# Performance work log

Hardware: AMD Instinct MI355X
Metric: run time of the kernel (lower is better)

## Reference

```python
import math
import jax, jax.numpy as jnp
import numpy as np

H = 16  # num_attention_heads
D = 64  # attention_head_size
ALPHA = 32.0  # PB-relax alpha


def setup_inputs() -> dict:
    key = jax.random.key(0)
    ks = jax.random.split(key, 8)
    B, S, C = 4, 1024, 1024
    scale = 1.0 / math.sqrt(C)
    return {
        "hidden_states": jax.random.normal(ks[0], (B, S, C), jnp.float32),
        "attention_mask": jnp.zeros((B, 1, 1, S), jnp.float32),
        "rel_pos": jax.random.normal(ks[1], (B, H, S, S), jnp.float32),
        "rel_2d_pos": jax.random.normal(ks[2], (B, H, S, S), jnp.float32),
        "Wq": jax.random.normal(ks[3], (C, C), jnp.float32) * scale,
        "bq": jnp.zeros((C,), jnp.float32),
        "Wk": jax.random.normal(ks[4], (C, C), jnp.float32) * scale,
        "bk": jnp.zeros((C,), jnp.float32),
        "Wv": jax.random.normal(ks[5], (C, C), jnp.float32) * scale,
        "bv": jnp.zeros((C,), jnp.float32),
    }


def _heads(x, B, S):
    # [B,S,C] -> [B,H,S,D]
    return x.reshape(B, S, H, D).transpose(0, 2, 1, 3)


def cogview_softmax(scores):
    # PB-relax: softmax(((s/alpha) - max(s/alpha)) * alpha)
    s = scores / ALPHA
    m = jnp.max(s, axis=-1, keepdims=True)
    return jax.nn.softmax((s - m) * ALPHA, axis=-1)


def reference(hidden_states, attention_mask, rel_pos, rel_2d_pos,
              Wq, bq, Wk, bk, Wv, bv):
    B, S, C = hidden_states.shape
    inv_sqrt_d = 1.0 / math.sqrt(D)
    # torch nn.Linear: y = x @ W.T + b; here W is stored as [out, in]
    q = _heads(hidden_states @ Wq.T + bq, B, S)  # [B,H,S,D]
    k = _heads(hidden_states @ Wk.T + bk, B, S)
    v = _heads(hidden_states @ Wv.T + bv, B, S)

    scores = jnp.einsum('bhqd,bhkd->bhqk', q * inv_sqrt_d, k)
    scores = scores + (rel_pos + rel_2d_pos) * inv_sqrt_d
    scores = scores + attention_mask  # broadcast [B,1,1,S]

    probs = cogview_softmax(scores)  # dropout prob = 0 (eval)
    ctx = jnp.einsum('bhqk,bhkd->bhqd', probs, v)
    ctx = ctx.transpose(0, 2, 1, 3).reshape(B, S, C)
    return ctx
```

## Files before the change

kernel.cpp:

```cpp
#include <hip/hip_runtime.h>
#include <hip/hip_bf16.h>

typedef __attribute__((ext_vector_type(8))) short bf16x8;
typedef __attribute__((ext_vector_type(4))) float f32x4;

#define LDSG(g, l) __builtin_amdgcn_global_load_lds(                      \
    (const __attribute__((address_space(1))) void*)(g),                   \
    (__attribute__((address_space(3))) void*)(l), 16, 0, 0)

#define LOG2E 1.44269504088896f
#define RELSC 0.180336880111112f

__global__ __launch_bounds__(256) void cvt_kernel(
    const float* __restrict__ hs,
    const float* __restrict__ wq, const float* __restrict__ wk,
    const float* __restrict__ wv,
    __hip_bfloat16* __restrict__ hbf, __hip_bfloat16* __restrict__ wbf)
{
  const int NH = (4 * 1024 * 1024) / 4;
  const int NW = (1024 * 1024) / 4;
  int i = blockIdx.x * 256 + threadIdx.x;
  float4 v;
  __hip_bfloat16* dst;
  if (i < NH) {
    v = ((const float4*)hs)[i];
    dst = hbf + (size_t)i * 4;
  } else {
    int j = i - NH;
    int which = j / NW, r = j - which * NW;
    const float* src = which == 0 ? wq : (which == 1 ? wk : wv);
    v = ((const float4*)src)[r];
    dst = wbf + (size_t)j * 4;
  }
  union { ushort4 u; __hip_bfloat16 b[4]; } o;
  o.b[0] = __float2bfloat16(v.x);
  o.b[1] = __float2bfloat16(v.y);
  o.b[2] = __float2bfloat16(v.z);
  o.b[3] = __float2bfloat16(v.w);
  *((ushort4*)dst) = o.u;
}

__global__ __launch_bounds__(256) void qkv_gemm(
    const __hip_bfloat16* __restrict__ A,
    const __hip_bfloat16* __restrict__ W,
    const float* __restrict__ bq, const float* __restrict__ bk,
    const float* __restrict__ bv,
    __hip_bfloat16* __restrict__ qo, __hip_bfloat16* __restrict__ ko,
    __hip_bfloat16* __restrict__ vo)
{
  const int K = 1024;
  __shared__ __hip_bfloat16 As[128 * 64];
  __shared__ __hip_bfloat16 Bs[128 * 64];
  const int bid = blockIdx.x;
  const int bm = bid & 31, bn = bid >> 5;
  const int m0 = bm * 128, n0 = bn * 128;
  const int tid = threadIdx.x, wid = tid >> 6, lane = tid & 63;
  const int wm = wid >> 1, wn = wid & 1;

  f32x4 acc[4][4] = {};

  const int srow = lane >> 3;
  const int schunk = (lane & 7) ^ srow;

  for (int k0 = 0; k0 < K; k0 += 64) {
#pragma unroll
    for (int p = 0; p < 4; ++p) {
      int r = (wid * 4 + p) * 8 + srow;
      LDSG(&A[(size_t)(m0 + r) * K + k0 + schunk * 8], &As[(wid * 4 + p) * 512]);
      LDSG(&W[(size_t)(n0 + r) * K + k0 + schunk * 8], &Bs[(wid * 4 + p) * 512]);
    }
    __syncthreads();
#pragma unroll
    for (int ks = 0; ks < 2; ++ks) {
      bf16x8 af[4], bfr[4];
#pragma unroll
      for (int mi = 0; mi < 4; ++mi) {
        int row = wm * 64 + mi * 16 + (lane & 15);
        int slot = (ks * 4 + (lane >> 4)) ^ (lane & 7);
        af[mi] = *(const bf16x8*)((const char*)As + row * 128 + slot * 16);
      }
#pragma unroll
      for (int ni = 0; ni < 4; ++ni) {
        int row = wn * 64 + ni * 16 + (lane & 15);
        int slot = (ks * 4 + (lane >> 4)) ^ (lane & 7);
        bfr[ni] = *(const bf16x8*)((const char*)Bs + row * 128 + slot * 16);
      }
#pragma unroll
      for (int mi = 0; mi < 4; ++mi)
#pragma unroll
        for (int ni = 0; ni < 4; ++ni)
          acc[mi][ni] = __builtin_amdgcn_mfma_f32_16x16x32_bf16(
              af[mi], bfr[ni], acc[mi][ni], 0, 0, 0);
    }
    __syncthreads();
  }

#pragma unroll
  for (int ni = 0; ni < 4; ++ni) {
    int n = n0 + wn * 64 + ni * 16 + (lane & 15);
    int which = n >> 10;
    int h = (n >> 6) & 15;
    int d = n & 63;
    const float* bias = which == 0 ? bq : (which == 1 ? bk : bv);
    float bval = bias[n & 1023];
    if (which == 2) {
#pragma unroll
      for (int mi = 0; mi < 4; ++mi) {
        int m = m0 + wm * 64 + mi * 16 + (lane >> 4) * 4;
        int b = m >> 10, s = m & 1023;
        union { ushort4 u; __hip_bfloat16 bb[4]; } o;
#pragma unroll
        for (int j = 0; j < 4; ++j)
          o.bb[j] = __float2bfloat16(acc[mi][ni][j] + bval);
        *(ushort4*)&vo[((size_t)((b * 16 + h) * 64 + d) << 10) + s] = o.u;
      }
    } else {
      __hip_bfloat16* dst = which == 0 ? qo : ko;
      float scale = (which == 0) ? RELSC : 1.0f;
#pragma unroll
      for (int mi = 0; mi < 4; ++mi) {
#pragma unroll
        for (int j = 0; j < 4; ++j) {
          int m = m0 + wm * 64 + mi * 16 + (lane >> 4) * 4 + j;
          int b = m >> 10, s = m & 1023;
          float val = (acc[mi][ni][j] + bval) * scale;
          dst[(((size_t)(b * 16 + h) << 10) + s) * 64 + d] = __float2bfloat16(val);
        }
      }
    }
  }
}

__global__ __launch_bounds__(256, 3) void attn_kernel(
    const __hip_bfloat16* __restrict__ qg, const __hip_bfloat16* __restrict__ kg,
    const __hip_bfloat16* __restrict__ vtg,
    const float* __restrict__ rel1, const float* __restrict__ rel2,
    const float* __restrict__ mask, float* __restrict__ out)
{
  __shared__ __hip_bfloat16 Ks[2][64 * 64];
  __shared__ __hip_bfloat16 Vts[2][64 * 64];
  __shared__ __hip_bfloat16 Ps[4][16 * 64];

  const int bid = blockIdx.x;
  const int bh = bid & 63, qt = bid >> 6;
  const int b = bh >> 4, h = bh & 15;
  const int tid = threadIdx.x, wid = tid >> 6, lane = tid & 63;
  const int lg = lane >> 4, ln15 = lane & 15;

  const size_t kvbase = (size_t)bh << 16;
  const int q0 = qt * 64 + wid * 16;

  bf16x8 qf[2];
  qf[0] = *(const bf16x8*)&qg[kvbase + (size_t)(q0 + ln15) * 64 + lg * 8];
  qf[1] = *(const bf16x8*)&qg[kvbase + (size_t)(q0 + ln15) * 64 + 32 + lg * 8];

  f32x4 accO[4] = {};
  float mrun = -1e30f, lrun = 0.f;

  const int srow = lane >> 3, sc8 = lane & 7;
  const float* relp1 = rel1 + ((size_t)bh << 20) + (size_t)(q0 + ln15) * 1024;
  const float* relp2 = rel2 + ((size_t)bh << 20) + (size_t)(q0 + ln15) * 1024;
  const float* maskp = mask + ((size_t)b << 10);

  float4 ra[2][2][4];

#define REL_LOAD(BUF, KB) do {                                              \
    _Pragma("unroll") for (int ct = 0; ct < 4; ++ct) {                      \
      ra[BUF][0][ct] = *(const float4*)&relp1[(KB) + ct * 16 + lg * 4];     \
      ra[BUF][1][ct] = *(const float4*)&relp2[(KB) + ct * 16 + lg * 4];     \
    } } while (0)

#define STAGE(BUF, KB) do {                                                 \
    _Pragma("unroll") for (int pp = 0; pp < 2; ++pp) {                      \
      int rr = (wid * 2 + pp) * 8 + srow;                                   \
      LDSG(&kg[kvbase + (size_t)((KB) + rr) * 64 + (sc8 ^ (rr & 7)) * 8],   \
           &Ks[BUF][(wid * 2 + pp) * 512]);                                 \
      LDSG(&vtg[kvbase + (size_t)rr * 1024 + (KB) + (sc8 ^ (rr & 7)) * 8],  \
           &Vts[BUF][(wid * 2 + pp) * 512]);                                \
    } } while (0)

#define BODY(CB, KT) do {                                                   \
    if ((KT) + 1 < 16) {                                                    \
      REL_LOAD((CB) ^ 1, ((KT) + 1) * 64);                                  \
      STAGE((CB) ^ 1, ((KT) + 1) * 64);                                     \
    }                                                                       \
    f32x4 st[4] = {};                                                       \
    _Pragma("unroll") for (int ks = 0; ks < 2; ++ks)                        \
      _Pragma("unroll") for (int ct = 0; ct < 4; ++ct) {                    \
        int row = ct * 16 + ln15;                                           \
        bf16x8 kf = *(const bf16x8*)((const char*)&Ks[CB][0] + row * 128 +  \
                                     (((ks * 4 + lg) ^ (row & 7)) * 16));   \
        st[ct] = __builtin_amdgcn_mfma_f32_16x16x32_bf16(kf, qf[ks], st[ct],\
                                                         0, 0, 0);          \
      }                                                                     \
    float p[4][4]; float mt = -1e30f;                                       \
    const int kb_ = (KT) * 64;                                              \
    _Pragma("unroll") for (int ct = 0; ct < 4; ++ct) {                      \
      float4 mv = *(const float4*)&maskp[kb_ + ct * 16 + lg * 4];           \
      _Pragma("unroll") for (int j = 0; j < 4; ++j) {                       \
        float sv = st[ct][j] +                                              \
                   RELSC * (((const float*)&ra[CB][0][ct])[j] +             \
                            ((const float*)&ra[CB][1][ct])[j]) +            \
                   LOG2E * ((const float*)&mv)[j];                          \
        p[ct][j] = sv; mt = fmaxf(mt, sv);                                  \
      }                                                                     \
    }                                                                       \
    mt = fmaxf(mt, __shfl_xor(mt, 16, 64));                                 \
    mt = fmaxf(mt, __shfl_xor(mt, 32, 64));                                 \
    float mnew = fmaxf(mrun, mt);                                           \
    float sc_ = __builtin_amdgcn_exp2f(mrun - mnew);                        \
    mrun = mnew;                                                            \
    float lsum = 0.f;                                                       \
    _Pragma("unroll") for (int ct = 0; ct < 4; ++ct)                        \
      _Pragma("unroll") for (int j = 0; j < 4; ++j) {                       \
        float e = __builtin_amdgcn_exp2f(p[ct][j] - mnew);                  \
        p[ct][j] = e; lsum += e;                                            \
      }                                                                     \
    lsum += __shfl_xor(lsum, 16, 64);                                       \
    lsum += __shfl_xor(lsum, 32, 64);                                       \
    lrun = lrun * sc_ + lsum;                                               \
    _Pragma("unroll") for (int dt = 0; dt < 4; ++dt) accO[dt] *= sc_;       \
    __hip_bfloat16* Pw = &Ps[wid][0];                                       \
    _Pragma("unroll") for (int ct = 0; ct < 4; ++ct) {                      \
      union { ushort4 u; __hip_bfloat16 bb[4]; } w;                         \
      _Pragma("unroll") for (int j = 0; j < 4; ++j)                         \
        w.bb[j] = __float2bfloat16(p[ct][j]);                               \
      *(ushort4*)((char*)Pw + ln15 * 128 +                                  \
                  ((ct * 32 + lg * 8) ^ ((ln15 & 7) << 4))) = w.u;          \
    }                                                                       \
    bf16x8 pt[2];                                                           \
    pt[0] = *(const bf16x8*)((const char*)Pw + ln15 * 128 +                 \
                             ((lg * 16) ^ ((ln15 & 7) << 4)));              \
    pt[1] = *(const bf16x8*)((const char*)Pw + ln15 * 128 +                 \
                             ((64 + lg * 16) ^ ((ln15 & 7) << 4)));         \
    _Pragma("unroll") for (int ks = 0; ks < 2; ++ks)                        \
      _Pragma("unroll") for (int dt = 0; dt < 4; ++dt) {                    \
        int drow = dt * 16 + ln15;                                          \
        bf16x8 vf = *(const bf16x8*)((const char*)&Vts[CB][0] + drow * 128 +\
                                     (((ks * 4 + lg) ^ (drow & 7)) * 16));  \
        accO[dt] = __builtin_amdgcn_mfma_f32_16x16x32_bf16(vf, pt[ks],      \
                                                           accO[dt], 0, 0, 0);\
      }                                                                     \
    __syncthreads();                                                        \
  } while (0)

  REL_LOAD(0, 0);
  STAGE(0, 0);
  __syncthreads();

  for (int t = 0; t < 8; ++t) {
    BODY(0, 2 * t);
    BODY(1, 2 * t + 1);
  }

  float rl = 1.0f / lrun;
#pragma unroll
  for (int dt = 0; dt < 4; ++dt) {
    float4 o;
    o.x = accO[dt][0] * rl;
    o.y = accO[dt][1] * rl;
    o.z = accO[dt][2] * rl;
    o.w = accO[dt][3] * rl;
    *(float4*)&out[((size_t)(b * 1024 + q0 + ln15)) * 1024 + h * 64 +
                   dt * 16 + lg * 4] = o;
  }
}

extern "C" void kernel_launch(void* const* d_in, const int* in_sizes, int n_in,
                              void* d_out, int out_size, void* d_ws,
                              size_t ws_size, hipStream_t stream) {
  const float* hs   = (const float*)d_in[0];
  const float* mask = (const float*)d_in[1];
  const float* rel1 = (const float*)d_in[2];
  const float* rel2 = (const float*)d_in[3];
  const float* Wq   = (const float*)d_in[4];
  const float* bq   = (const float*)d_in[5];
  const float* Wk   = (const float*)d_in[6];
  const float* bk   = (const float*)d_in[7];
  const float* Wv   = (const float*)d_in[8];
  const float* bv   = (const float*)d_in[9];

  char* ws = (char*)d_ws;
  __hip_bfloat16* hbf = (__hip_bfloat16*)(ws);
  __hip_bfloat16* wbf = (__hip_bfloat16*)(ws + 8388608);
  __hip_bfloat16* qb  = (__hip_bfloat16*)(ws + 14680064);
  __hip_bfloat16* kb  = (__hip_bfloat16*)(ws + 23068672);
  __hip_bfloat16* vtb = (__hip_bfloat16*)(ws + 31457280);

  cvt_kernel<<<7168, 256, 0, stream>>>(hs, Wq, Wk, Wv, hbf, wbf);
  qkv_gemm<<<768, 256, 0, stream>>>(hbf, wbf, bq, bk, bv, qb, kb, vtb);
  attn_kernel<<<1024, 256, 0, stream>>>(qb, kb, vtb, rel1, rel2, mask,
                                        (float*)d_out);
}
```

Before: 205.6 us.

## Use single-wave attention blocks loading K and V directly into registers

The attention kernel changes from 4-wave blocks with K and V staged through LDS to 64-thread blocks, each handling 16 query rows. K and V fragments now come straight from global memory into registers, with K and the relative-position bias register double-buffered across tiles. This removes LDS staging and the per-tile __syncthreads. The cost is that each wave fetches its own copy of K and V instead of sharing it, which raises global and L2 traffic and register pressure.

```diff
diff --git a/kernel.cpp b/kernel.cpp
--- a/kernel.cpp
+++ b/kernel.cpp
@@ -131,24 +131,22 @@
   }
 }
 
-__global__ __launch_bounds__(256, 3) void attn_kernel(
+__global__ __launch_bounds__(64, 2) void attn_kernel(
     const __hip_bfloat16* __restrict__ qg, const __hip_bfloat16* __restrict__ kg,
     const __hip_bfloat16* __restrict__ vtg,
     const float* __restrict__ rel1, const float* __restrict__ rel2,
     const float* __restrict__ mask, float* __restrict__ out)
 {
-  __shared__ __hip_bfloat16 Ks[2][64 * 64];
-  __shared__ __hip_bfloat16 Vts[2][64 * 64];
-  __shared__ __hip_bfloat16 Ps[4][16 * 64];
+  __shared__ __hip_bfloat16 Ps[16 * 64];
 
   const int bid = blockIdx.x;
   const int bh = bid & 63, qt = bid >> 6;
   const int b = bh >> 4, h = bh & 15;
-  const int tid = threadIdx.x, wid = tid >> 6, lane = tid & 63;
+  const int lane = threadIdx.x;
   const int lg = lane >> 4, ln15 = lane & 15;
 
   const size_t kvbase = (size_t)bh << 16;
-  const int q0 = qt * 64 + wid * 16;
+  const int q0 = qt * 16;
 
   bf16x8 qf[2];
   qf[0] = *(const bf16x8*)&qg[kvbase + (size_t)(q0 + ln15) * 64 + lg * 8];
@@ -157,50 +155,49 @@
   f32x4 accO[4] = {};
   float mrun = -1e30f, lrun = 0.f;
 
-  const int srow = lane >> 3, sc8 = lane & 7;
   const float* relp1 = rel1 + ((size_t)bh << 20) + (size_t)(q0 + ln15) * 1024;
   const float* relp2 = rel2 + ((size_t)bh << 20) + (size_t)(q0 + ln15) * 1024;
   const float* maskp = mask + ((size_t)b << 10);
 
-  float4 ra[2][2][4];
-
-#define REL_LOAD(BUF, KB) do {                                              \
+#define LOAD_REL(R1, R2, KBO) do {                                          \
     _Pragma("unroll") for (int ct = 0; ct < 4; ++ct) {                      \
-      ra[BUF][0][ct] = *(const float4*)&relp1[(KB) + ct * 16 + lg * 4];     \
-      ra[BUF][1][ct] = *(const float4*)&relp2[(KB) + ct * 16 + lg * 4];     \
+      R1[ct] = *(const float4*)&relp1[(KBO) + ct * 16 + lg * 4];            \
+      R2[ct] = *(const float4*)&relp2[(KBO) + ct * 16 + lg * 4];            \
     } } while (0)
 
-#define STAGE(BUF, KB) do {                                                 \
-    _Pragma("unroll") for (int pp = 0; pp < 2; ++pp) {                      \
-      int rr = (wid * 2 + pp) * 8 + srow;                                   \
-      LDSG(&kg[kvbase + (size_t)((KB) + rr) * 64 + (sc8 ^ (rr & 7)) * 8],   \
-           &Ks[BUF][(wid * 2 + pp) * 512]);                                 \
-      LDSG(&vtg[kvbase + (size_t)rr * 1024 + (KB) + (sc8 ^ (rr & 7)) * 8],  \
-           &Vts[BUF][(wid * 2 + pp) * 512]);                                \
-    } } while (0)
-
-#define BODY(CB, KT) do {                                                   \
-    if ((KT) + 1 < 16) {                                                    \
-      REL_LOAD((CB) ^ 1, ((KT) + 1) * 64);                                  \
-      STAGE((CB) ^ 1, ((KT) + 1) * 64);                                     \
+#define LOAD_K(KF, KBO) do {                                                \
+    _Pragma("unroll") for (int ks = 0; ks < 2; ++ks)                        \
+      _Pragma("unroll") for (int ct = 0; ct < 4; ++ct)                      \
+        KF[ks * 4 + ct] = *(const bf16x8*)&kg[kvbase +                      \
+            (size_t)((KBO) + ct * 16 + ln15) * 64 + ks * 32 + lg * 8];      \
+    } while (0)
+
+#define LOAD_V(VF, KBO) do {                                                \
+    _Pragma("unroll") for (int ks = 0; ks < 2; ++ks)                        \
+      _Pragma("unroll") for (int dt = 0; dt < 4; ++dt)                      \
+        VF[ks * 4 + dt] = *(const bf16x8*)&vtg[kvbase +                     \
+            (size_t)(dt * 16 + ln15) * 1024 + (KBO) + ks * 32 + lg * 8];    \
+    } while (0)
+
+#define BODY(RC1, RC2, KC, RN1, RN2, KN, KT) do {                           \
+    bf16x8 vfr[8];                                                          \
+    LOAD_V(vfr, (KT) * 64);                                                 \
+    if ((KT) < 15) {                                                        \
+      LOAD_REL(RN1, RN2, ((KT) + 1) * 64);                                  \
+      LOAD_K(KN, ((KT) + 1) * 64);                                          \
     }                                                                       \
     f32x4 st[4] = {};                                                       \
     _Pragma("unroll") for (int ks = 0; ks < 2; ++ks)                        \
-      _Pragma("unroll") for (int ct = 0; ct < 4; ++ct) {                    \
-        int row = ct * 16 + ln15;                                           \
-        bf16x8 kf = *(const bf16x8*)((const char*)&Ks[CB][0] + row * 128 +  \
-                                     (((ks * 4 + lg) ^ (row & 7)) * 16));   \
-        st[ct] = __builtin_amdgcn_mfma_f32_16x16x32_bf16(kf, qf[ks], st[ct],\
-                                                         0, 0, 0);          \
-      }                                                                     \
+      _Pragma("unroll") for (int ct = 0; ct < 4; ++ct)                      \
+        st[ct] = __builtin_amdgcn_mfma_f32_16x16x32_bf16(                   \
+            KC[ks * 4 + ct], qf[ks], st[ct], 0, 0, 0);                      \
     float p[4][4]; float mt = -1e30f;                                       \
-    const int kb_ = (KT) * 64;                                              \
     _Pragma("unroll") for (int ct = 0; ct < 4; ++ct) {                      \
-      float4 mv = *(const float4*)&maskp[kb_ + ct * 16 + lg * 4];           \
+      float4 mv = *(const float4*)&maskp[(KT) * 64 + ct * 16 + lg * 4];     \
       _Pragma("unroll") for (int j = 0; j < 4; ++j) {                       \
         float sv = st[ct][j] +                                              \
-                   RELSC * (((const float*)&ra[CB][0][ct])[j] +             \
-                            ((const float*)&ra[CB][1][ct])[j]) +            \
+                   RELSC * (((const float*)&RC1[ct])[j] +                   \
+                            ((const float*)&RC2[ct])[j]) +                  \
                    LOG2E * ((const float*)&mv)[j];                          \
         p[ct][j] = sv; mt = fmaxf(mt, sv);                                  \
       }                                                                     \
@@ -220,37 +217,34 @@
     lsum += __shfl_xor(lsum, 32, 64);                                       \
     lrun = lrun * sc_ + lsum;                                               \
     _Pragma("unroll") for (int dt = 0; dt < 4; ++dt) accO[dt] *= sc_;       \
-    __hip_bfloat16* Pw = &Ps[wid][0];                                       \
     _Pragma("unroll") for (int ct = 0; ct < 4; ++ct) {                      \
       union { ushort4 u; __hip_bfloat16 bb[4]; } w;                         \
       _Pragma("unroll") for (int j = 0; j < 4; ++j)                         \
         w.bb[j] = __float2bfloat16(p[ct][j]);                               \
-      *(ushort4*)((char*)Pw + ln15 * 128 +                                  \
+      *(ushort4*)((char*)Ps + ln15 * 128 +                                  \
                   ((ct * 32 + lg * 8) ^ ((ln15 & 7) << 4))) = w.u;          \
     }                                                                       \
     bf16x8 pt[2];                                                           \
-    pt[0] = *(const bf16x8*)((const char*)Pw + ln15 * 128 +                 \
+    pt[0] = *(const bf16x8*)((const char*)Ps + ln15 * 128 +                 \
                              ((lg * 16) ^ ((ln15 & 7) << 4)));              \
-    pt[1] = *(const bf16x8*)((const char*)Pw + ln15 * 128 +                 \
+    pt[1] = *(const bf16x8*)((const char*)Ps + ln15 * 128 +                 \
                              ((64 + lg * 16) ^ ((ln15 & 7) << 4)));         \
     _Pragma("unroll") for (int ks = 0; ks < 2; ++ks)                        \
-      _Pragma("unroll") for (int dt = 0; dt < 4; ++dt) {                    \
-        int drow = dt * 16 + ln15;                                          \
-        bf16x8 vf = *(const bf16x8*)((const char*)&Vts[CB][0] + drow * 128 +\
-                                     (((ks * 4 + lg) ^ (drow & 7)) * 16));  \
-        accO[dt] = __builtin_amdgcn_mfma_f32_16x16x32_bf16(vf, pt[ks],      \
-                                                           accO[dt], 0, 0, 0);\
-      }                                                                     \
-    __syncthreads();                                                        \
+      _Pragma("unroll") for (int dt = 0; dt < 4; ++dt)                      \
+        accO[dt] = __builtin_amdgcn_mfma_f32_16x16x32_bf16(                 \
+            vfr[ks * 4 + dt], pt[ks], accO[dt], 0, 0, 0);                   \
   } while (0)
 
-  REL_LOAD(0, 0);
-  STAGE(0, 0);
-  __syncthreads();
-
+  float4 r1a[4], r2a[4], r1b[4], r2b[4];
+  bf16x8 kfa[8], kfb[8];
+
+  LOAD_REL(r1a, r2a, 0);
+  LOAD_K(kfa, 0);
+
+#pragma unroll
   for (int t = 0; t < 8; ++t) {
-    BODY(0, 2 * t);
-    BODY(1, 2 * t + 1);
+    BODY(r1a, r2a, kfa, r1b, r2b, kfb, 2 * t);
+    BODY(r1b, r2b, kfb, r1a, r2a, kfa, 2 * t + 1);
   }
 
   float rl = 1.0f / lrun;
@@ -289,6 +283,6 @@
 
   cvt_kernel<<<7168, 256, 0, stream>>>(hs, Wq, Wk, Wv, hbf, wbf);
   qkv_gemm<<<768, 256, 0, stream>>>(hbf, wbf, bq, bk, bv, qb, kb, vtb);
-  attn_kernel<<<1024, 256, 0, stream>>>(qb, kb, vtb, rel1, rel2, mask,
-                                        (float*)d_out);
-}
+  attn_kernel<<<4096, 64, 0, stream>>>(qb, kb, vtb, rel1, rel2, mask,
+                                       (float*)d_out);
+}
```

Result: slower. 335.0 us (+62.9%).
